# Kernel tuning notes

Hardware: AMD Instinct MI355X
Metric: run time of the kernel (lower is better)

## Reference

```python
import jax, jax.numpy as jnp
import numpy as np

C = 512
HEADS = 8
HEAD_DIM = C // HEADS
GROUPS = 32
EPS = 1e-5


def group_norm(x, scale, bias):
    b, c, h, w = x.shape
    xg = x.reshape(b, GROUPS, -1)
    mean = xg.mean(axis=-1, keepdims=True)
    var = xg.var(axis=-1, keepdims=True)
    xg = (xg - mean) * jax.lax.rsqrt(var + EPS)
    x = xg.reshape(b, c, h, w)
    return x * scale[None, :, None, None] + bias[None, :, None, None]


def conv1x1(x, w, b):
    # w: (out_c, in_c), x: (B, C, H, W)
    return jnp.einsum('oc,bchw->bohw', w, x) + b[None, :, None, None]


def setup_inputs() -> dict:
    key = jax.random.key(0)
    ks = jax.random.split(key, 11)
    s = 1.0 / np.sqrt(C)
    return {
        'x': jax.random.normal(ks[0], (8, C, 32, 32), jnp.float32),
        'gn_scale': jnp.ones((C,), jnp.float32),
        'gn_bias': jnp.zeros((C,), jnp.float32),
        'wq': jax.random.normal(ks[1], (C, C), jnp.float32) * s,
        'bq': jax.random.normal(ks[2], (C,), jnp.float32) * 0.01,
        'wk': jax.random.normal(ks[3], (C, C), jnp.float32) * s,
        'bk': jax.random.normal(ks[4], (C,), jnp.float32) * 0.01,
        'wv': jax.random.normal(ks[5], (C, C), jnp.float32) * s,
        'bv': jax.random.normal(ks[6], (C,), jnp.float32) * 0.01,
        'wp': jax.random.normal(ks[7], (C, C), jnp.float32) * s,
        'bp': jax.random.normal(ks[8], (C,), jnp.float32) * 0.01,
    }


def reference(x, gn_scale, gn_bias, wq, bq, wk, bk, wv, bv, wp, bp):
    b, c, h, w = x.shape
    n = h * w
    h_in = x
    xn = group_norm(x, gn_scale, gn_bias)
    q = conv1x1(xn, wq, bq).reshape(b, HEADS, HEAD_DIM, n)
    k = conv1x1(xn, wk, bk).reshape(b, HEADS, HEAD_DIM, n)
    v = conv1x1(xn, wv, bv).reshape(b, HEADS, HEAD_DIM, n)
    scale = 1.0 / np.sqrt(HEAD_DIM).astype(np.float32)
    attn = jnp.einsum('bhcn,bhcm->bhnm', q, k) * scale
    attn = jax.nn.softmax(attn, axis=-1)
    out = jnp.einsum('bhnm,bhcm->bhcn', attn, v)
    out = out.reshape(b, c, h, w)
    out = conv1x1(out, wp, bp)
    return out + h_in
```

## Files before the change

kernel.cpp:

```cpp
#include <hip/hip_runtime.h>

#define CC 512
#define NN 1024
#define NB 8
#define NH 8
#define HD 64

typedef __attribute__((ext_vector_type(8))) short s16x8;
typedef __attribute__((ext_vector_type(4))) short s16x4;
typedef __attribute__((ext_vector_type(4))) float f32x4;
typedef __attribute__((ext_vector_type(16))) float f32x16;

__device__ __forceinline__ short f2bf(float f){
  union { float f; unsigned u; } v; v.f = f;
  unsigned r = v.u + 0x7fffu + ((v.u >> 16) & 1u);
  return (short)(r >> 16);
}

__device__ __forceinline__ unsigned cvtpk(float lo, float hi){
  unsigned r;
  asm("v_cvt_pk_bf16_f32 %0, %1, %2" : "=v"(r) : "v"(lo), "v"(hi));
  return r;
}

__device__ __forceinline__ void gload16(const void* g, void* l){
  __builtin_amdgcn_global_load_lds((const __attribute__((address_space(1))) void*)g,
                                   (__attribute__((address_space(3))) void*)l, 16, 0, 0);
}

__global__ __launch_bounds__(256) void prep_kernel(const float* __restrict__ x,
    const float* __restrict__ gsc, const float* __restrict__ gbi,
    const float* __restrict__ w0, const float* __restrict__ w1,
    const float* __restrict__ w2, const float* __restrict__ w3,
    short* __restrict__ wbf, short* __restrict__ xnt){
  if (blockIdx.x < 1024){
    const int i = blockIdx.x*256 + threadIdx.x;
    const int sel = i >> 16;
    const int off = (i & 65535) << 2;
    const float* src = (sel==0) ? w0 : (sel==1) ? w1 : (sel==2) ? w2 : w3;
    const float4 v = *reinterpret_cast<const float4*>(src + off);
    s16x4 o;
    o[0] = f2bf(v.x); o[1] = f2bf(v.y); o[2] = f2bf(v.z); o[3] = f2bf(v.w);
    *reinterpret_cast<s16x4*>(wbf + (size_t)sel*262144 + off) = o;
    return;
  }
  const int blk = blockIdx.x - 1024;
  const int b = blk >> 5;
  const int g = blk & 31;
  const int t = threadIdx.x;
  const float* base = x + ((size_t)b*CC + g*16)*NN;
  float4 vals[16];
  float s = 0.f, s2 = 0.f;
  #pragma unroll
  for (int k = 0; k < 16; ++k){
    float4 v = *reinterpret_cast<const float4*>(base + k*NN + t*4);
    vals[k] = v;
    s  += v.x + v.y + v.z + v.w;
    s2 += v.x*v.x + v.y*v.y + v.z*v.z + v.w*v.w;
  }
  #pragma unroll
  for (int m = 1; m < 64; m <<= 1){ s += __shfl_xor(s, m); s2 += __shfl_xor(s2, m); }
  __shared__ float rs[4], rs2[4];
  const int wid = t >> 6, lane = t & 63;
  if (lane == 0){ rs[wid] = s; rs2[wid] = s2; }
  __syncthreads();
  s  = rs[0] + rs[1] + rs[2] + rs[3];
  s2 = rs2[0] + rs2[1] + rs2[2] + rs2[3];
  const float mean = s * (1.f/16384.f);
  const float inv = rsqrtf(s2 * (1.f/16384.f) - mean*mean + 1e-5f);
  float scl[16], off[16];
  #pragma unroll
  for (int k = 0; k < 16; ++k){
    const float sc = gsc[g*16 + k] * inv;
    scl[k] = sc;
    off[k] = gbi[g*16 + k] - mean * sc;
  }
  short* obase = xnt + ((size_t)b*NN + t*4)*CC + g*16;
  #pragma unroll
  for (int i = 0; i < 4; ++i){
    s16x8 lo, hi;
    #pragma unroll
    for (int k = 0; k < 8; ++k){
      float v = (i==0) ? vals[k].x : (i==1) ? vals[k].y : (i==2) ? vals[k].z : vals[k].w;
      lo[k] = f2bf(v * scl[k] + off[k]);
    }
    #pragma unroll
    for (int k = 0; k < 8; ++k){
      float v = (i==0) ? vals[k+8].x : (i==1) ? vals[k+8].y : (i==2) ? vals[k+8].z : vals[k+8].w;
      hi[k] = f2bf(v * scl[k+8] + off[k+8]);
    }
    *reinterpret_cast<s16x8*>(obase + (size_t)i*CC)     = lo;
    *reinterpret_cast<s16x8*>(obase + (size_t)i*CC + 8) = hi;
  }
}

template<int MODE>
__global__ __launch_bounds__(256) void gemm_kernel(
    const short* __restrict__ Wb, const short* __restrict__ Bmat,
    const float* __restrict__ bias0, const float* __restrict__ bias1, const float* __restrict__ bias2,
    const float* __restrict__ resid,
    short* __restrict__ qt, short* __restrict__ kt2, short* __restrict__ vo,
    float* __restrict__ outp)
{
  const int w = blockIdx.x;
  const int nt = w & 7;
  const int s = w >> 3;
  const int batch = s & 7;
  int mt, z;
  if (MODE == 0){ const int r = s >> 3; mt = r & 3; z = r >> 2; }
  else          { mt = s >> 3; z = 0; }
  const int tid = threadIdx.x;
  const int lane = tid & 63, wid = tid >> 6;
  const int wm = wid >> 1, wn = wid & 1;

  __shared__ short As[128*64];
  __shared__ short Bs[128*64];

  const short* Wz = Wb + (size_t)(MODE == 0 ? z : 3) * 262144;
  const short* Brow = Bmat + ((size_t)batch*NN + nt*128)*CC;

  const f32x4 fzero = {0.f, 0.f, 0.f, 0.f};
  f32x4 acc[4][4];
  #pragma unroll
  for (int i = 0; i < 4; ++i)
  #pragma unroll
  for (int j = 0; j < 4; ++j)
    acc[i][j] = fzero;

  for (int kk = 0; kk < 8; ++kk){
    __syncthreads();
    #pragma unroll
    for (int j = 0; j < 4; ++j){
      const int id = tid + 256*j;
      const int row = id >> 3, ch = id & 7;
      const int gch = ch ^ (row & 7);
      gload16(Wz   + (size_t)(mt*128 + row)*CC + kk*64 + gch*8, As + (wid*64 + 256*j)*8);
      gload16(Brow + (size_t)row*CC          + kk*64 + gch*8, Bs + (wid*64 + 256*j)*8);
    }
    __syncthreads();
    #pragma unroll
    for (int ks = 0; ks < 2; ++ks){
      s16x8 a[4], b[4];
      #pragma unroll
      for (int mi = 0; mi < 4; ++mi){
        const int row = wm*64 + mi*16 + (lane & 15);
        const int ch = (ks*4 + (lane >> 4)) ^ (row & 7);
        a[mi] = *reinterpret_cast<const s16x8*>(&As[row*64 + ch*8]);
      }
      #pragma unroll
      for (int ni = 0; ni < 4; ++ni){
        const int row = wn*64 + ni*16 + (lane & 15);
        const int ch = (ks*4 + (lane >> 4)) ^ (row & 7);
        b[ni] = *reinterpret_cast<const s16x8*>(&Bs[row*64 + ch*8]);
      }
      if (MODE == 0 && z == 2){
        #pragma unroll
        for (int mi = 0; mi < 4; ++mi)
        #pragma unroll
        for (int ni = 0; ni < 4; ++ni)
          acc[mi][ni] = __builtin_amdgcn_mfma_f32_16x16x32_bf16(b[ni], a[mi], acc[mi][ni], 0, 0, 0);
      } else {
        #pragma unroll
        for (int mi = 0; mi < 4; ++mi)
        #pragma unroll
        for (int ni = 0; ni < 4; ++ni)
          acc[mi][ni] = __builtin_amdgcn_mfma_f32_16x16x32_bf16(a[mi], b[ni], acc[mi][ni], 0, 0, 0);
      }
    }
  }

  const int obase = mt*128 + wm*64;
  const int nbase = nt*128 + wn*64;
  if (MODE == 0){
    const int head = mt*2 + wm;
    const size_t hb = ((size_t)batch*NH + head)*65536;
    const int hi2 = (lane >> 5) & 1;
    const int j0 = ((lane >> 4) & 1)*4;
    if (z < 2){
      const float* bias = (z == 0) ? bias0 : bias1;
      short* dst = (z == 0) ? qt : kt2;
      const float qs = (z == 0) ? 0.125f * 1.44269504f : 1.0f;
      #pragma unroll
      for (int mi = 0; mi < 4; ++mi){
        float bv4[4];
        #pragma unroll
        for (int r = 0; r < 4; ++r) bv4[r] = bias[obase + mi*16 + (lane>>4)*4 + r];
        #pragma unroll
        for (int ni = 0; ni < 4; ++ni){
          const int l = (ni & 1)*16 + (lane & 15) + 32*hi2;
          const int q5 = nt*4 + wn*2 + (ni >> 1);
          s16x4 pk;
          #pragma unroll
          for (int r = 0; r < 4; ++r) pk[r] = f2bf((acc[mi][ni][r] + bv4[r]) * qs);
          *reinterpret_cast<s16x4*>(dst + hb + (size_t)((q5*4 + mi)*64 + l)*8 + j0) = pk;
        }
      }
    } else {
      #pragma unroll
      for (int mi = 0; mi < 4; ++mi){
        const float bv = bias2[obase + mi*16 + (lane & 15)];
        const int ci = mi >> 1;
        const int cl = (mi & 1)*16 + (lane & 15);
        #pragma unroll
        for (int ni = 0; ni < 4; ++ni){
          const int m5 = nt*2 + wn;
          s16x4 pk;
          #pragma unroll
          for (int r = 0; r < 4; ++r) pk[r] = f2bf(acc[mi][ni][r] + bv);
          *reinterpret_cast<s16x4*>(vo + hb + (size_t)((((ci*16 + m5)*4 + ni)*64) + cl + 32*hi2)*8 + j0) = pk;
        }
      }
    }
  } else {
    #pragma unroll
    for (int mi = 0; mi < 4; ++mi){
      float bv4[4];
      #pragma unroll
      for (int r = 0; r < 4; ++r) bv4[r] = bias0[obase + mi*16 + (lane>>4)*4 + r];
      #pragma unroll
      for (int ni = 0; ni < 4; ++ni){
        const int n = nbase + ni*16 + (lane & 15);
        #pragma unroll
        for (int r = 0; r < 4; ++r){
          const int o = obase + mi*16 + (lane>>4)*4 + r;
          const size_t idx = ((size_t)batch*CC + o)*NN + n;
          outp[idx] = acc[mi][ni][r] + bv4[r] + resid[idx];
        }
      }
    }
  }
}

__global__ __launch_bounds__(256, 2) void attn_kernel(
    const short* __restrict__ qp, const short* __restrict__ kp, const short* __restrict__ vp,
    short* __restrict__ ot)
{
  const int bid = blockIdx.x;
  const int xcd = bid & 7, rr = bid >> 3;
  const int bh  = xcd*8 + (rr & 7);
  const int qt  = rr >> 3;
  const int b = bh >> 3, head = bh & 7;
  const int tid = threadIdx.x, lane = tid & 63, wid = tid >> 6;
  const int col = lane & 31;
  const int qg = wid & 1, kh = wid >> 1;
  const int q0 = qt*64 + qg*32;

  const short* Qf = qp + (size_t)bh*65536;
  const short* Kf = kp + (size_t)bh*65536;
  const short* Vf = vp + (size_t)bh*65536;

  __shared__ float Lof[2][32][64];
  __shared__ float Lm[2][64];
  __shared__ float Ll[2][64];

  const int q5 = qt*2 + qg;
  s16x8 qf[4];
  #pragma unroll
  for (int ks = 0; ks < 4; ++ks)
    qf[ks] = *reinterpret_cast<const s16x8*>(Qf + (size_t)(q5*4 + ks)*512 + lane*8);

  f32x16 of0, of1;
  #pragma unroll
  for (int r = 0; r < 16; ++r){ of0[r] = 0.f; of1[r] = 0.f; }
  float m = -1e30f, l = 0.f;

  auto kload = [&](int itn, s16x8 (&kf)[2][4]){
    const short* kb = Kf + (size_t)(kh*16 + itn*2)*2048 + lane*8;
    #pragma unroll
    for (int t = 0; t < 2; ++t)
      #pragma unroll
      for (int ks = 0; ks < 4; ++ks)
        kf[t][ks] = *reinterpret_cast<const s16x8*>(kb + t*2048 + ks*512);
  };

  auto pack = [&](f32x16& sv, s16x8& p0, s16x8& p1){
    union { unsigned u[4]; s16x8 v; } w0, w1;
    {
      unsigned a = cvtpk(sv[0], sv[1]);
      unsigned c = cvtpk(sv[4], sv[5]);
      auto r = __builtin_amdgcn_permlane32_swap(a, c, false, false);
      w0.u[0] = r[0]; w0.u[2] = r[1];
      a = cvtpk(sv[2], sv[3]);
      c = cvtpk(sv[6], sv[7]);
      r = __builtin_amdgcn_permlane32_swap(a, c, false, false);
      w0.u[1] = r[0]; w0.u[3] = r[1];
    }
    {
      unsigned a = cvtpk(sv[8], sv[9]);
      unsigned c = cvtpk(sv[12], sv[13]);
      auto r = __builtin_amdgcn_permlane32_swap(a, c, false, false);
      w1.u[0] = r[0]; w1.u[2] = r[1];
      a = cvtpk(sv[10], sv[11]);
      c = cvtpk(sv[14], sv[15]);
      r = __builtin_amdgcn_permlane32_swap(a, c, false, false);
      w1.u[1] = r[0]; w1.u[3] = r[1];
    }
    p0 = w0.v; p1 = w1.v;
  };

  auto body = [&](int it, s16x8 (&kf)[2][4], s16x8 (&kfn)[2][4]){
    const int m5 = kh*8 + it;
    s16x8 vf[2][4];
    const short* vb = Vf + (size_t)m5*2048 + lane*8;
    #pragma unroll
    for (int ci = 0; ci < 2; ++ci)
      #pragma unroll
      for (int s = 0; s < 4; ++s)
        vf[ci][s] = *reinterpret_cast<const s16x8*>(vb + ci*32768 + s*512);
    f32x16 s0, s1;
    #pragma unroll
    for (int r = 0; r < 16; ++r){ s0[r] = 0.f; s1[r] = 0.f; }
    #pragma unroll
    for (int ks = 0; ks < 4; ++ks){
      s0 = __builtin_amdgcn_mfma_f32_32x32x16_bf16(kf[0][ks], qf[ks], s0, 0, 0, 0);
      s1 = __builtin_amdgcn_mfma_f32_32x32x16_bf16(kf[1][ks], qf[ks], s1, 0, 0, 0);
    }
    if (it < 7) kload(it + 1, kfn);
    float t[16];
    #pragma unroll
    for (int r = 0; r < 16; ++r) t[r] = fmaxf(s0[r], s1[r]);
    #pragma unroll
    for (int o = 8; o > 0; o >>= 1)
      #pragma unroll
      for (int r = 0; r < 8; ++r) if (r < o) t[r] = fmaxf(t[r], t[r + o]);
    float tm = fmaxf(t[0], __shfl_xor(t[0], 32));
    const float mn = fmaxf(m, tm);
    const float sc = __builtin_amdgcn_exp2f(m - mn);
    m = mn;
    #pragma unroll
    for (int r = 0; r < 16; ++r){ s0[r] = __builtin_amdgcn_exp2f(s0[r] - mn); }
    #pragma unroll
    for (int r = 0; r < 16; ++r){ s1[r] = __builtin_amdgcn_exp2f(s1[r] - mn); }
    #pragma unroll
    for (int r = 0; r < 16; ++r) t[r] = s0[r] + s1[r];
    #pragma unroll
    for (int o = 8; o > 0; o >>= 1)
      #pragma unroll
      for (int r = 0; r < 8; ++r) if (r < o) t[r] = t[r] + t[r + o];
    float rs = t[0] + __shfl_xor(t[0], 32);
    l = l*sc + rs;
    #pragma unroll
    for (int r = 0; r < 16; ++r){ of0[r] *= sc; of1[r] *= sc; }
    s16x8 pf[4];
    pack(s0, pf[0], pf[1]);
    pack(s1, pf[2], pf[3]);
    #pragma unroll
    for (int s = 0; s < 4; ++s){
      of0 = __builtin_amdgcn_mfma_f32_32x32x16_bf16(vf[0][s], pf[s], of0, 0, 0, 0);
      of1 = __builtin_amdgcn_mfma_f32_32x32x16_bf16(vf[1][s], pf[s], of1, 0, 0, 0);
    }
  };

  s16x8 kfA[2][4], kfB[2][4];
  kload(0, kfA);
  #pragma unroll 1
  for (int ii = 0; ii < 4; ++ii){
    body(2*ii,     kfA, kfB);
    body(2*ii + 1, kfB, kfA);
  }

  __syncthreads();
  if (kh == 1){
    #pragma unroll
    for (int r = 0; r < 16; ++r){
      Lof[qg][r][lane]      = of0[r];
      Lof[qg][16 + r][lane] = of1[r];
    }
    Lm[qg][lane] = m;
    Ll[qg][lane] = l;
  }
  __syncthreads();
  if (kh == 0){
    const float m1 = Lm[qg][lane], l1 = Ll[qg][lane];
    const float mn = fmaxf(m, m1);
    const float a0 = __builtin_amdgcn_exp2f(m - mn);
    const float a1 = __builtin_amdgcn_exp2f(m1 - mn);
    const float linv = 1.f / (l*a0 + l1*a1);
    const int hi = lane >> 5;
    const int n = q0 + col;
    short* ob = ot + ((size_t)b*NN + n)*CC + head*HD + hi*4;
    #pragma unroll
    for (int rq = 0; rq < 4; ++rq){
      s16x4 pk;
      #pragma unroll
      for (int r = 0; r < 4; ++r)
        pk[r] = f2bf((of0[rq*4 + r]*a0 + Lof[qg][rq*4 + r][lane]*a1) * linv);
      *reinterpret_cast<s16x4*>(ob + rq*8) = pk;
      #pragma unroll
      for (int r = 0; r < 4; ++r)
        pk[r] = f2bf((of1[rq*4 + r]*a0 + Lof[qg][16 + rq*4 + r][lane]*a1) * linv);
      *reinterpret_cast<s16x4*>(ob + 32 + rq*8) = pk;
    }
  }
}

extern "C" void kernel_launch(void* const* d_in, const int* in_sizes, int n_in,
                              void* d_out, int out_size, void* d_ws, size_t ws_size,
                              hipStream_t stream) {
  const float* x   = (const float*)d_in[0];
  const float* gsc = (const float*)d_in[1];
  const float* gbi = (const float*)d_in[2];
  const float* wq  = (const float*)d_in[3];
  const float* bq  = (const float*)d_in[4];
  const float* wk  = (const float*)d_in[5];
  const float* bk  = (const float*)d_in[6];
  const float* wv  = (const float*)d_in[7];
  const float* bv  = (const float*)d_in[8];
  const float* wp  = (const float*)d_in[9];
  const float* bp  = (const float*)d_in[10];
  float* out = (float*)d_out;

  char* ws = (char*)d_ws;
  short* wbf = (short*)(ws);
  short* xnt = (short*)(ws + (2u<<20));
  short* qt  = (short*)(ws + (10u<<20));
  short* kt  = (short*)(ws + (18u<<20));
  short* v   = (short*)(ws + (26u<<20));
  short* aot = (short*)(ws + (34u<<20));

  prep_kernel<<<1280, 256, 0, stream>>>(x, gsc, gbi, wq, wk, wv, wp, wbf, xnt);
  gemm_kernel<0><<<dim3(768), 256, 0, stream>>>(wbf, xnt, bq, bk, bv, nullptr,
                                                qt, kt, v, nullptr);
  attn_kernel<<<dim3(1024), 256, 0, stream>>>(qt, kt, v, aot);
  gemm_kernel<1><<<dim3(256), 256, 0, stream>>>(wbf, aot, bp, nullptr, nullptr, x,
                                                nullptr, nullptr, nullptr, out);
}
```

Before: 81.05 us.

## Process two batches per QKV GEMM block and use packed bf16 conversion

The QKV projection GEMM now has each block compute two batches, loading the shared weight tile once and reusing it across both activation tiles. This halves the grid to 384 blocks and cuts weight traffic. In exchange, the block needs twice the accumulator registers and more LDS, which may reduce occupancy. Separately, scalar software float-to-bf16 rounding is replaced with the hardware v_cvt_pk_bf16_f32 packed conversion in the prep, GEMM epilogue and attention output paths.

```diff
diff --git a/kernel.cpp b/kernel.cpp
--- a/kernel.cpp
+++ b/kernel.cpp
@@ -21,6 +21,13 @@
   unsigned r;
   asm("v_cvt_pk_bf16_f32 %0, %1, %2" : "=v"(r) : "v"(lo), "v"(hi));
   return r;
+}
+
+__device__ __forceinline__ s16x4 pack4(float a, float b, float c, float d){
+  union { unsigned u[2]; s16x4 v; } r;
+  r.u[0] = cvtpk(a, b);
+  r.u[1] = cvtpk(c, d);
+  return r.v;
 }
 
 __device__ __forceinline__ void gload16(const void* g, void* l){
@@ -39,9 +46,7 @@
     const int off = (i & 65535) << 2;
     const float* src = (sel==0) ? w0 : (sel==1) ? w1 : (sel==2) ? w2 : w3;
     const float4 v = *reinterpret_cast<const float4*>(src + off);
-    s16x4 o;
-    o[0] = f2bf(v.x); o[1] = f2bf(v.y); o[2] = f2bf(v.z); o[3] = f2bf(v.w);
-    *reinterpret_cast<s16x4*>(wbf + (size_t)sel*262144 + off) = o;
+    *reinterpret_cast<s16x4*>(wbf + (size_t)sel*262144 + off) = pack4(v.x, v.y, v.z, v.w);
     return;
   }
   const int blk = blockIdx.x - 1024;
@@ -78,19 +83,20 @@
   short* obase = xnt + ((size_t)b*NN + t*4)*CC + g*16;
   #pragma unroll
   for (int i = 0; i < 4; ++i){
-    s16x8 lo, hi;
-    #pragma unroll
-    for (int k = 0; k < 8; ++k){
-      float v = (i==0) ? vals[k].x : (i==1) ? vals[k].y : (i==2) ? vals[k].z : vals[k].w;
-      lo[k] = f2bf(v * scl[k] + off[k]);
-    }
-    #pragma unroll
-    for (int k = 0; k < 8; ++k){
-      float v = (i==0) ? vals[k+8].x : (i==1) ? vals[k+8].y : (i==2) ? vals[k+8].z : vals[k+8].w;
-      hi[k] = f2bf(v * scl[k+8] + off[k+8]);
-    }
-    *reinterpret_cast<s16x8*>(obase + (size_t)i*CC)     = lo;
-    *reinterpret_cast<s16x8*>(obase + (size_t)i*CC + 8) = hi;
+    float fv[16];
+    #pragma unroll
+    for (int k = 0; k < 16; ++k){
+      const float v = (i==0) ? vals[k].x : (i==1) ? vals[k].y : (i==2) ? vals[k].z : vals[k].w;
+      fv[k] = v * scl[k] + off[k];
+    }
+    union { unsigned u[4]; s16x8 v; } lo, hi;
+    #pragma unroll
+    for (int j = 0; j < 4; ++j){
+      lo.u[j] = cvtpk(fv[2*j],     fv[2*j + 1]);
+      hi.u[j] = cvtpk(fv[8 + 2*j], fv[8 + 2*j + 1]);
+    }
+    *reinterpret_cast<s16x8*>(obase + (size_t)i*CC)     = lo.v;
+    *reinterpret_cast<s16x8*>(obase + (size_t)i*CC + 8) = hi.v;
   }
 }
 
@@ -102,30 +108,32 @@
     short* __restrict__ qt, short* __restrict__ kt2, short* __restrict__ vo,
     float* __restrict__ outp)
 {
+  constexpr int NPB = (MODE == 0) ? 2 : 1;
   const int w = blockIdx.x;
   const int nt = w & 7;
   const int s = w >> 3;
-  const int batch = s & 7;
-  int mt, z;
-  if (MODE == 0){ const int r = s >> 3; mt = r & 3; z = r >> 2; }
-  else          { mt = s >> 3; z = 0; }
+  int mt, z, b0;
+  if (MODE == 0){ const int bp = s & 3; const int r = s >> 2; mt = r & 3; z = r >> 2; b0 = bp*2; }
+  else          { b0 = s & 7; mt = s >> 3; z = 0; }
   const int tid = threadIdx.x;
   const int lane = tid & 63, wid = tid >> 6;
   const int wm = wid >> 1, wn = wid & 1;
 
   __shared__ short As[128*64];
-  __shared__ short Bs[128*64];
+  __shared__ short Bs[NPB][128*64];
 
   const short* Wz = Wb + (size_t)(MODE == 0 ? z : 3) * 262144;
-  const short* Brow = Bmat + ((size_t)batch*NN + nt*128)*CC;
+  const short* B0row = Bmat + ((size_t)b0*NN + nt*128)*CC;
 
   const f32x4 fzero = {0.f, 0.f, 0.f, 0.f};
-  f32x4 acc[4][4];
+  f32x4 acc[NPB][4][4];
+  #pragma unroll
+  for (int p = 0; p < NPB; ++p)
   #pragma unroll
   for (int i = 0; i < 4; ++i)
   #pragma unroll
   for (int j = 0; j < 4; ++j)
-    acc[i][j] = fzero;
+    acc[p][i][j] = fzero;
 
   for (int kk = 0; kk < 8; ++kk){
     __syncthreads();
@@ -134,13 +142,16 @@
       const int id = tid + 256*j;
       const int row = id >> 3, ch = id & 7;
       const int gch = ch ^ (row & 7);
-      gload16(Wz   + (size_t)(mt*128 + row)*CC + kk*64 + gch*8, As + (wid*64 + 256*j)*8);
-      gload16(Brow + (size_t)row*CC          + kk*64 + gch*8, Bs + (wid*64 + 256*j)*8);
+      const int dst = (wid*64 + 256*j)*8;
+      gload16(Wz + (size_t)(mt*128 + row)*CC + kk*64 + gch*8, As + dst);
+      #pragma unroll
+      for (int p = 0; p < NPB; ++p)
+        gload16(B0row + (size_t)p*NN*CC + (size_t)row*CC + kk*64 + gch*8, &Bs[p][dst]);
     }
     __syncthreads();
     #pragma unroll
     for (int ks = 0; ks < 2; ++ks){
-      s16x8 a[4], b[4];
+      s16x8 a[4];
       #pragma unroll
       for (int mi = 0; mi < 4; ++mi){
         const int row = wm*64 + mi*16 + (lane & 15);
@@ -148,23 +159,27 @@
         a[mi] = *reinterpret_cast<const s16x8*>(&As[row*64 + ch*8]);
       }
       #pragma unroll
-      for (int ni = 0; ni < 4; ++ni){
-        const int row = wn*64 + ni*16 + (lane & 15);
-        const int ch = (ks*4 + (lane >> 4)) ^ (row & 7);
-        b[ni] = *reinterpret_cast<const s16x8*>(&Bs[row*64 + ch*8]);
-      }
-      if (MODE == 0 && z == 2){
+      for (int p = 0; p < NPB; ++p){
+        s16x8 b[4];
         #pragma unroll
-        for (int mi = 0; mi < 4; ++mi)
-        #pragma unroll
-        for (int ni = 0; ni < 4; ++ni)
-          acc[mi][ni] = __builtin_amdgcn_mfma_f32_16x16x32_bf16(b[ni], a[mi], acc[mi][ni], 0, 0, 0);
-      } else {
-        #pragma unroll
-        for (int mi = 0; mi < 4; ++mi)
-        #pragma unroll
-        for (int ni = 0; ni < 4; ++ni)
-          acc[mi][ni] = __builtin_amdgcn_mfma_f32_16x16x32_bf16(a[mi], b[ni], acc[mi][ni], 0, 0, 0);
+        for (int ni = 0; ni < 4; ++ni){
+          const int row = wn*64 + ni*16 + (lane & 15);
+          const int ch = (ks*4 + (lane >> 4)) ^ (row & 7);
+          b[ni] = *reinterpret_cast<const s16x8*>(&Bs[p][row*64 + ch*8]);
+        }
+        if (MODE == 0 && z == 2){
+          #pragma unroll
+          for (int mi = 0; mi < 4; ++mi)
+          #pragma unroll
+          for (int ni = 0; ni < 4; ++ni)
+            acc[p][mi][ni] = __builtin_amdgcn_mfma_f32_16x16x32_bf16(b[ni], a[mi], acc[p][mi][ni], 0, 0, 0);
+        } else {
+          #pragma unroll
+          for (int mi = 0; mi < 4; ++mi)
+          #pragma unroll
+          for (int ni = 0; ni < 4; ++ni)
+            acc[p][mi][ni] = __builtin_amdgcn_mfma_f32_16x16x32_bf16(a[mi], b[ni], acc[p][mi][ni], 0, 0, 0);
+        }
       }
     }
   }
@@ -173,41 +188,45 @@
   const int nbase = nt*128 + wn*64;
   if (MODE == 0){
     const int head = mt*2 + wm;
-    const size_t hb = ((size_t)batch*NH + head)*65536;
     const int hi2 = (lane >> 5) & 1;
     const int j0 = ((lane >> 4) & 1)*4;
-    if (z < 2){
-      const float* bias = (z == 0) ? bias0 : bias1;
-      short* dst = (z == 0) ? qt : kt2;
-      const float qs = (z == 0) ? 0.125f * 1.44269504f : 1.0f;
-      #pragma unroll
-      for (int mi = 0; mi < 4; ++mi){
-        float bv4[4];
+    #pragma unroll
+    for (int p = 0; p < NPB; ++p){
+      const int batch = b0 + p;
+      const size_t hb = ((size_t)batch*NH + head)*65536;
+      if (z < 2){
+        const float* bias = (z == 0) ? bias0 : bias1;
+        short* dst = (z == 0) ? qt : kt2;
+        const float qs = (z == 0) ? 0.125f * 1.44269504f : 1.0f;
         #pragma unroll
-        for (int r = 0; r < 4; ++r) bv4[r] = bias[obase + mi*16 + (lane>>4)*4 + r];
+        for (int mi = 0; mi < 4; ++mi){
+          float bv4[4];
+          #pragma unroll
+          for (int r = 0; r < 4; ++r) bv4[r] = bias[obase + mi*16 + (lane>>4)*4 + r];
+          #pragma unroll
+          for (int ni = 0; ni < 4; ++ni){
+            const int l = (ni & 1)*16 + (lane & 15) + 32*hi2;
+            const int q5 = nt*4 + wn*2 + (ni >> 1);
+            const s16x4 pk = pack4((acc[p][mi][ni][0] + bv4[0]) * qs,
+                                   (acc[p][mi][ni][1] + bv4[1]) * qs,
+                                   (acc[p][mi][ni][2] + bv4[2]) * qs,
+                                   (acc[p][mi][ni][3] + bv4[3]) * qs);
+            *reinterpret_cast<s16x4*>(dst + hb + (size_t)((q5*4 + mi)*64 + l)*8 + j0) = pk;
+          }
+        }
+      } else {
         #pragma unroll
-        for (int ni = 0; ni < 4; ++ni){
-          const int l = (ni & 1)*16 + (lane & 15) + 32*hi2;
-          const int q5 = nt*4 + wn*2 + (ni >> 1);
-          s16x4 pk;
-          #pragma unroll
-          for (int r = 0; r < 4; ++r) pk[r] = f2bf((acc[mi][ni][r] + bv4[r]) * qs);
-          *reinterpret_cast<s16x4*>(dst + hb + (size_t)((q5*4 + mi)*64 + l)*8 + j0) = pk;
-        }
-      }
-    } else {
-      #pragma unroll
-      for (int mi = 0; mi < 4; ++mi){
-        const float bv = bias2[obase + mi*16 + (lane & 15)];
-        const int ci = mi >> 1;
-        const int cl = (mi & 1)*16 + (lane & 15);
-        #pragma unroll
-        for (int ni = 0; ni < 4; ++ni){
-          const int m5 = nt*2 + wn;
-          s16x4 pk;
-          #pragma unroll
-          for (int r = 0; r < 4; ++r) pk[r] = f2bf(acc[mi][ni][r] + bv);
-          *reinterpret_cast<s16x4*>(vo + hb + (size_t)((((ci*16 + m5)*4 + ni)*64) + cl + 32*hi2)*8 + j0) = pk;
+        for (int mi = 0; mi < 4; ++mi){
+          const float bv = bias2[obase + mi*16 + (lane & 15)];
+          const int ci = mi >> 1;
+          const int cl = (mi & 1)*16 + (lane & 15);
+          #pragma unroll
+          for (int ni = 0; ni < 4; ++ni){
+            const int m5 = nt*2 + wn;
+            const s16x4 pk = pack4(acc[p][mi][ni][0] + bv, acc[p][mi][ni][1] + bv,
+                                   acc[p][mi][ni][2] + bv, acc[p][mi][ni][3] + bv);
+            *reinterpret_cast<s16x4*>(vo + hb + (size_t)((((ci*16 + m5)*4 + ni)*64) + cl + 32*hi2)*8 + j0) = pk;
+          }
         }
       }
     }
@@ -223,8 +242,8 @@
         #pragma unroll
         for (int r = 0; r < 4; ++r){
           const int o = obase + mi*16 + (lane>>4)*4 + r;
-          const size_t idx = ((size_t)batch*CC + o)*NN + n;
-          outp[idx] = acc[mi][ni][r] + bv4[r] + resid[idx];
+          const size_t idx = ((size_t)b0*CC + o)*NN + n;
+          outp[idx] = acc[0][mi][ni][r] + bv4[r] + resid[idx];
         }
       }
     }
@@ -381,14 +400,15 @@
     short* ob = ot + ((size_t)b*NN + n)*CC + head*HD + hi*4;
     #pragma unroll
     for (int rq = 0; rq < 4; ++rq){
-      s16x4 pk;
-      #pragma unroll
-      for (int r = 0; r < 4; ++r)
-        pk[r] = f2bf((of0[rq*4 + r]*a0 + Lof[qg][rq*4 + r][lane]*a1) * linv);
+      s16x4 pk = pack4((of0[rq*4 + 0]*a0 + Lof[qg][rq*4 + 0][lane]*a1) * linv,
+                       (of0[rq*4 + 1]*a0 + Lof[qg][rq*4 + 1][lane]*a1) * linv,
+                       (of0[rq*4 + 2]*a0 + Lof[qg][rq*4 + 2][lane]*a1) * linv,
+                       (of0[rq*4 + 3]*a0 + Lof[qg][rq*4 + 3][lane]*a1) * linv);
       *reinterpret_cast<s16x4*>(ob + rq*8) = pk;
-      #pragma unroll
-      for (int r = 0; r < 4; ++r)
-        pk[r] = f2bf((of1[rq*4 + r]*a0 + Lof[qg][16 + rq*4 + r][lane]*a1) * linv);
+      pk = pack4((of1[rq*4 + 0]*a0 + Lof[qg][16 + rq*4 + 0][lane]*a1) * linv,
+                 (of1[rq*4 + 1]*a0 + Lof[qg][16 + rq*4 + 1][lane]*a1) * linv,
+                 (of1[rq*4 + 2]*a0 + Lof[qg][16 + rq*4 + 2][lane]*a1) * linv,
+                 (of1[rq*4 + 3]*a0 + Lof[qg][16 + rq*4 + 3][lane]*a1) * linv);
       *reinterpret_cast<s16x4*>(ob + 32 + rq*8) = pk;
     }
   }
@@ -419,7 +439,7 @@
   short* aot = (short*)(ws + (34u<<20));
 
   prep_kernel<<<1280, 256, 0, stream>>>(x, gsc, gbi, wq, wk, wv, wp, wbf, xnt);
-  gemm_kernel<0><<<dim3(768), 256, 0, stream>>>(wbf, xnt, bq, bk, bv, nullptr,
+  gemm_kernel<0><<<dim3(384), 256, 0, stream>>>(wbf, xnt, bq, bk, bv, nullptr,
                                                 qt, kt, v, nullptr);
   attn_kernel<<<dim3(1024), 256, 0, stream>>>(qt, kt, v, aot);
   gemm_kernel<1><<<dim3(256), 256, 0, stream>>>(wbf, aot, bp, nullptr, nullptr, x,
```

Result: slower. 86.75 us (+7.0%).
